# Performance work log

Hardware: AMD Instinct MI355X
Metric: run time of the kernel (lower is better)

Reference implementation:

```python
import jax, jax.numpy as jnp
import numpy as np

B, S, D, H = 4, 2048, 1024, 16
HD = D // H  # head_dim = 64


def setup_inputs() -> dict:
    key = jax.random.key(0)
    ks = jax.random.split(key, 5)
    scale = 0.02
    return {
        "x": jax.random.normal(ks[0], (B, S, D), dtype=jnp.float32),
        "Wq": jax.random.normal(ks[1], (D, D), dtype=jnp.float32) * scale,
        "Wk": jax.random.normal(ks[2], (D, D), dtype=jnp.float32) * scale,
        "Wv": jax.random.normal(ks[3], (D, D), dtype=jnp.float32) * scale,
        "Wo": jax.random.normal(ks[4], (D, D), dtype=jnp.float32) * scale,
        "bo": jnp.zeros((D,), dtype=jnp.float32),
    }


def reference(x, Wq, Wk, Wv, Wo, bo):
    b, s, d = x.shape
    # projections (no bias on q/k/v, matching qkv_bias=False)
    q = (x @ Wq).reshape(b, s, H, HD).transpose(0, 2, 1, 3)  # [B,H,S,HD]
    k = (x @ Wk).reshape(b, s, H, HD).transpose(0, 2, 1, 3)
    v = (x @ Wv).reshape(b, s, H, HD).transpose(0, 2, 1, 3)
    scores = jnp.einsum("bhqd,bhkd->bhqk", q, k) / jnp.sqrt(jnp.float32(HD))
    causal = jnp.tril(jnp.ones((s, s), dtype=bool))  # True = keep
    scores = jnp.where(causal, scores, -jnp.inf)
    attn = jax.nn.softmax(scores, axis=-1)
    # dropout p=0.0 -> identity
    out = jnp.einsum("bhqk,bhkd->bhqd", attn, v)
    out = out.transpose(0, 2, 1, 3).reshape(b, s, d)
    return out @ Wo + bo
```

## Files before the change

### kernel.cpp

```cpp
#include <hip/hip_runtime.h>

typedef unsigned short u16;
typedef unsigned int u32;
typedef __attribute__((ext_vector_type(4))) float f32x4;
typedef __attribute__((ext_vector_type(16))) float f32x16;
typedef __attribute__((ext_vector_type(8))) __bf16 bf16x8;
typedef __attribute__((ext_vector_type(4))) _Float16 f16x4;
typedef __attribute__((ext_vector_type(8))) _Float16 f16x8;
typedef __attribute__((ext_vector_type(4))) u16 u16x4;
typedef __attribute__((ext_vector_type(4))) u32 u32x4;
typedef __attribute__((ext_vector_type(2))) u32 u32x2;

#define D_ 1024
#define S_ 2048
#define B_ 4
#define H_ 16
#define HD_ 64
#define M_ 8192
#define LDP 72
#define QSCALE 0.18033688011112042591f

__device__ __forceinline__ u16 f2bf(float f) {
  u32 u = __float_as_uint(f);
  u += 0x7fffu + ((u >> 16) & 1u);
  return (u16)(u >> 16);
}

__device__ __forceinline__ float max3f(float a, float b, float c) {
  return fmaxf(fmaxf(a, b), c);
}

__device__ __forceinline__ void gload_lds16(const void* g, void* l) {
  __builtin_amdgcn_global_load_lds((const __attribute__((address_space(1))) void*)g,
                                   (__attribute__((address_space(3))) void*)l, 16, 0, 0);
}

__global__ __launch_bounds__(256) void prep_kernel(const float* __restrict__ x, u16* __restrict__ xb,
                                                   const float* __restrict__ Wq, const float* __restrict__ Wk,
                                                   const float* __restrict__ Wv, const float* __restrict__ Wo,
                                                   u16* __restrict__ Wqt, u16* __restrict__ Wkt,
                                                   u16* __restrict__ Wvt, u16* __restrict__ Wot) {
  __shared__ float lds[64][65];
  int lin = blockIdx.x;
  if (lin < 8192) {
    int i = (lin * 256 + threadIdx.x) * 4;
    f32x4 v = *(const f32x4*)(x + i);
    u16x4 o = {f2bf(v[0]), f2bf(v[1]), f2bf(v[2]), f2bf(v[3])};
    *(u16x4*)(xb + i) = o;
    return;
  }
  int pos = lin - 8192;
  int z = pos >> 8, rem = pos & 255;
  const float* W = z == 0 ? Wq : z == 1 ? Wk : z == 2 ? Wv : Wo;
  u16* Wt       = z == 0 ? Wqt : z == 1 ? Wkt : z == 2 ? Wvt : Wot;
  int k0 = (rem >> 4) * 64, n0 = (rem & 15) * 64;
  int tr = threadIdx.x >> 6, tc = threadIdx.x & 63;
#pragma unroll
  for (int i = 0; i < 16; ++i)
    lds[tr + i * 4][tc] = W[(size_t)(k0 + tr + i * 4) * D_ + n0 + tc];
  __syncthreads();
#pragma unroll
  for (int i = 0; i < 16; ++i)
    Wt[(size_t)(n0 + tr + i * 4) * D_ + k0 + tc] = f2bf(lds[tc][tr + i * 4]);
}

__device__ __forceinline__ void gemm_main(const u16* __restrict__ A, const u16* __restrict__ Bt,
                                          u16* As, u16* Bs, int row0, int col0, f32x4 acc[4][4]) {
  const int tid = threadIdx.x;
  const int lane = tid & 63, wave = tid >> 6;
  const int wr = wave >> 1, wc = wave & 1;
  const int l15 = lane & 15, lg = lane >> 4;
  const int sr8 = lane >> 3;
  const int scx = (lane & 7) ^ sr8;
#pragma unroll 1
  for (int k0 = 0; k0 < D_; k0 += 64) {
#pragma unroll
    for (int it = 0; it < 4; ++it) {
      int rbase = (it * 4 + wave) * 8;
      int r = rbase + sr8;
      gload_lds16(A + (size_t)(row0 + r) * D_ + k0 + scx * 8, As + rbase * 64);
      gload_lds16(Bt + (size_t)(col0 + r) * D_ + k0 + scx * 8, Bs + rbase * 64);
    }
    __syncthreads();
#pragma unroll
    for (int kk = 0; kk < 64; kk += 32) {
      const int cb = kk >> 3;
      bf16x8 af[4], bf[4];
#pragma unroll
      for (int m = 0; m < 4; ++m) {
        int row = wr * 64 + m * 16 + l15;
        af[m] = *(const bf16x8*)(As + row * 64 + (((cb + lg) ^ (l15 & 7)) << 3));
      }
#pragma unroll
      for (int n = 0; n < 4; ++n) {
        int row = wc * 64 + n * 16 + l15;
        bf[n] = *(const bf16x8*)(Bs + row * 64 + (((cb + lg) ^ (l15 & 7)) << 3));
      }
#pragma unroll
      for (int m = 0; m < 4; ++m)
#pragma unroll
        for (int n = 0; n < 4; ++n)
          acc[m][n] = __builtin_amdgcn_mfma_f32_16x16x32_bf16(af[m], bf[n], acc[m][n], 0, 0, 0);
    }
    __syncthreads();
  }
}

__global__ __launch_bounds__(256) void qkv_gemm_kernel(const u16* __restrict__ xb,
                                                       const u16* __restrict__ Wqt, const u16* __restrict__ Wkt,
                                                       const u16* __restrict__ Wvt,
                                                       u16* __restrict__ Qb, u16* __restrict__ Kb,
                                                       _Float16* __restrict__ Vt) {
  __shared__ u16 As[128 * 64];
  __shared__ u16 Bs[128 * 64];
  int lin = blockIdx.x;
  int xcd = lin & 7, pos = lin >> 3;
  int mode = pos / 64;
  int rem = pos & 63;
  int by = xcd * 8 + (rem >> 3);
  int bx = rem & 7;
  const u16* Bt = mode == 0 ? Wqt : mode == 1 ? Wkt : Wvt;
  f32x4 acc[4][4] = {};
  int row0 = by * 128, col0 = bx * 128;
  gemm_main(xb, Bt, As, Bs, row0, col0, acc);
  int lane = threadIdx.x & 63, wave = threadIdx.x >> 6;
  int wr = wave >> 1, wc = wave & 1, l15 = lane & 15, lg = lane >> 4;
  int rbase = row0 + wr * 64 + lg * 4, cbase = col0 + wc * 64 + l15;
  if (mode == 2) {
#pragma unroll
    for (int m = 0; m < 4; ++m) {
      int row = rbase + m * 16;
      int b = row >> 11, s = row & (S_ - 1);
#pragma unroll
      for (int n = 0; n < 4; ++n) {
        int col = cbase + n * 16;
        int h = col >> 6, hd = col & 63;
        f16x4 vv = {(_Float16)acc[m][n][0], (_Float16)acc[m][n][1],
                    (_Float16)acc[m][n][2], (_Float16)acc[m][n][3]};
        *(f16x4*)(Vt + ((size_t)((b << 4) + h) * HD_ + hd) * S_ + s) = vv;
      }
    }
  } else {
    u16* dst = mode == 0 ? Qb : Kb;
    float scl = mode == 0 ? QSCALE : 1.0f;
#pragma unroll
    for (int m = 0; m < 4; ++m)
#pragma unroll
      for (int n = 0; n < 4; ++n) {
        int col = cbase + n * 16;
#pragma unroll
        for (int r = 0; r < 4; ++r) {
          int row = rbase + m * 16 + r;
          dst[(size_t)row * D_ + col] = f2bf(acc[m][n][r] * scl);
        }
      }
  }
}

__global__ __launch_bounds__(128) void attn_kernel(const u16* __restrict__ Qb, const u16* __restrict__ Kb,
                                                   const _Float16* __restrict__ Vt, u16* __restrict__ attnb) {
  __shared__ u16 Ks[64][LDP];
  __shared__ _Float16 Vs[64][LDP];
  const int tid = threadIdx.x;
  const int wave = tid >> 6, lane = tid & 63;
  const int l31 = lane & 31, hi = lane >> 5;
  const int lin = blockIdx.x;
  const int xcd = lin & 7, slot = lin >> 3;
  const int qblk = 31 - (slot >> 3);
  const int bh = (slot & 7) * 8 + xcd;
  const int b = bh >> 4, h = bh & 15;
  const int ntiles = qblk + 1;
  const int wq0 = qblk * 64 + wave * 32;
  const int qg = wq0 + l31;

  const int srow = tid >> 1;
  const int sh = (tid & 1) * 32;
  const u16* Kp = Kb + (size_t)(b * S_ + srow) * D_ + h * HD_ + sh;
  const _Float16* Vp = Vt + ((size_t)bh * HD_ + srow) * S_ + sh;

  const u16* Qrow = Qb + (size_t)(b * S_ + qg) * D_ + h * HD_;
  bf16x8 qf[4];
#pragma unroll
  for (int ds = 0; ds < 4; ++ds)
    qf[ds] = *(const bf16x8*)(Qrow + ds * 16 + hi * 8);

  float m = -1e30f;
  f32x16 oL = {}, oH = {};
  f32x16 osum = {};
  const f16x8 ones8 = {(_Float16)1.f, (_Float16)1.f, (_Float16)1.f, (_Float16)1.f,
                       (_Float16)1.f, (_Float16)1.f, (_Float16)1.f, (_Float16)1.f};
  u32x4 kst[4], vst[4];

  auto tile_body = [&](int kvb, bool domask) {
    f32x16 sA = {}, sB = {};
    __builtin_amdgcn_s_setprio(1);
#pragma unroll
    for (int ds = 0; ds < 4; ++ds) {
      bf16x8 k0 = *(const bf16x8*)(&Ks[l31][ds * 16 + hi * 8]);
      bf16x8 k1 = *(const bf16x8*)(&Ks[32 + l31][ds * 16 + hi * 8]);
      sA = __builtin_amdgcn_mfma_f32_32x32x16_bf16(k0, qf[ds], sA, 0, 0, 0);
      sB = __builtin_amdgcn_mfma_f32_32x32x16_bf16(k1, qf[ds], sB, 0, 0, 0);
    }
    __builtin_amdgcn_s_setprio(0);
    if (domask) {
#pragma unroll
      for (int r = 0; r < 16; ++r) {
        int off = (r & 3) + 8 * (r >> 2) + 4 * hi;
        if (kvb + off > qg) sA[r] = -1e30f;
        if (kvb + 32 + off > qg) sB[r] = -1e30f;
      }
    }
    float mx[16];
#pragma unroll
    for (int r = 0; r < 16; ++r) mx[r] = fmaxf(sA[r], sB[r]);
    float y0 = max3f(mx[0], mx[1], mx[2]);
    float y1 = max3f(mx[3], mx[4], mx[5]);
    float y2 = max3f(mx[6], mx[7], mx[8]);
    float y3 = max3f(mx[9], mx[10], mx[11]);
    float y4 = max3f(mx[12], mx[13], mx[14]);
    float tmax = fmaxf(max3f(y0, y1, y2), max3f(y3, y4, mx[15]));
    tmax = fmaxf(tmax, __shfl_xor(tmax, 32));
    if (!__all(tmax - m <= 8.f)) {
      float nm = fmaxf(m, tmax);
      float alpha = exp2f(m - nm);
      m = nm;
      osum *= alpha;
      oL *= alpha;
      oH *= alpha;
    }
#pragma unroll
    for (int r = 0; r < 16; ++r) {
      sA[r] = exp2f(sA[r] - m);
      sB[r] = exp2f(sB[r] - m);
    }
    u32 uA[8], uB[8], vA[8], vB[8];
#pragma unroll
    for (int k = 0; k < 8; ++k) {
      uA[k] = __builtin_bit_cast(u32, __builtin_amdgcn_cvt_pkrtz(sA[2 * k], sA[2 * k + 1]));
      uB[k] = __builtin_bit_cast(u32, __builtin_amdgcn_cvt_pkrtz(sB[2 * k], sB[2 * k + 1]));
    }
#pragma unroll
    for (int k = 0; k < 8; ++k) {
      vA[k] = __shfl_xor(uA[k], 32);
      vB[k] = __shfl_xor(uB[k], 32);
    }
    __builtin_amdgcn_s_setprio(1);
#pragma unroll
    for (int ks = 0; ks < 4; ++ks) {
      const u32* U = (ks >> 1) ? uB : uA;
      const u32* Vw = (ks >> 1) ? vB : vA;
      const int b4 = (ks & 1) * 4;
      u32 w0 = hi ? Vw[b4 + 2] : U[b4 + 0];
      u32 w1 = hi ? Vw[b4 + 3] : U[b4 + 1];
      u32 w2 = hi ? U[b4 + 2] : Vw[b4 + 0];
      u32 w3 = hi ? U[b4 + 3] : Vw[b4 + 1];
      f16x8 pa = __builtin_bit_cast(f16x8, (u32x4){w0, w1, w2, w3});
      f16x8 v0 = *(const f16x8*)(&Vs[l31][ks * 16 + hi * 8]);
      f16x8 v1 = *(const f16x8*)(&Vs[32 + l31][ks * 16 + hi * 8]);
      oL = __builtin_amdgcn_mfma_f32_32x32x16_f16(v0, pa, oL, 0, 0, 0);
      oH = __builtin_amdgcn_mfma_f32_32x32x16_f16(v1, pa, oH, 0, 0, 0);
      osum = __builtin_amdgcn_mfma_f32_32x32x16_f16(ones8, pa, osum, 0, 0, 0);
    }
    __builtin_amdgcn_s_setprio(0);
  };

#pragma unroll
  for (int c = 0; c < 4; ++c) {
    kst[c] = *(const u32x4*)(Kp + c * 8);
    vst[c] = *(const u32x4*)(Vp + c * 8);
  }
  Kp += (size_t)64 * D_;
  Vp += 64;

#pragma unroll 1
  for (int t = 0; t < ntiles - 1; ++t) {
    __syncthreads();
#pragma unroll
    for (int c = 0; c < 4; ++c) {
      *(u32x4*)(&Ks[srow][sh + c * 8]) = kst[c];
      *(u32x4*)(&Vs[srow][sh + c * 8]) = vst[c];
    }
    __syncthreads();
#pragma unroll
    for (int c = 0; c < 4; ++c) {
      kst[c] = *(const u32x4*)(Kp + c * 8);
      vst[c] = *(const u32x4*)(Vp + c * 8);
    }
    Kp += (size_t)64 * D_;
    Vp += 64;
    tile_body(t * 64, false);
  }

  __syncthreads();
#pragma unroll
  for (int c = 0; c < 4; ++c) {
    *(u32x4*)(&Ks[srow][sh + c * 8]) = kst[c];
    *(u32x4*)(&Vs[srow][sh + c * 8]) = vst[c];
  }
  __syncthreads();
  tile_body((ntiles - 1) * 64, true);

  float inv = 1.0f / osum[0];
  __syncthreads();
  u16* scr = &Ks[wave * 32 + l31][0];
#pragma unroll
  for (int a = 0; a < 4; ++a) {
    u16x4 pl = {f2bf(oL[4 * a + 0] * inv), f2bf(oL[4 * a + 1] * inv),
                f2bf(oL[4 * a + 2] * inv), f2bf(oL[4 * a + 3] * inv)};
    *(u16x4*)(scr + 8 * a + 4 * hi) = pl;
    u16x4 ph = {f2bf(oH[4 * a + 0] * inv), f2bf(oH[4 * a + 1] * inv),
                f2bf(oH[4 * a + 2] * inv), f2bf(oH[4 * a + 3] * inv)};
    *(u16x4*)(scr + 32 + 8 * a + 4 * hi) = ph;
  }
  asm volatile("s_waitcnt lgkmcnt(0)" ::: "memory");
  const u16* srd = &Ks[wave * 32 + l31][hi * 32];
  u16* Og = attnb + (size_t)(b * S_ + wq0 + l31) * D_ + h * HD_ + hi * 32;
#pragma unroll
  for (int c = 0; c < 4; ++c)
    *(u32x4*)(Og + c * 8) = *(const u32x4*)(srd + c * 8);
}

__global__ __launch_bounds__(256) void out_gemm_kernel(const u16* __restrict__ attnb, const u16* __restrict__ Wot,
                                                       const float* __restrict__ bo, float* __restrict__ outp) {
  __shared__ u16 As[128 * 64];
  __shared__ u16 Bs[128 * 64];
  int lin = blockIdx.x;
  int xcd = lin & 7, pos = lin >> 3;
  int by = xcd * 8 + (pos >> 3);
  int bx = pos & 7;
  f32x4 acc[4][4] = {};
  int row0 = by * 128, col0 = bx * 128;
  gemm_main(attnb, Wot, As, Bs, row0, col0, acc);
  int lane = threadIdx.x & 63, wave = threadIdx.x >> 6;
  int wr = wave >> 1, wc = wave & 1, l15 = lane & 15, lg = lane >> 4;
  int rbase = row0 + wr * 64 + lg * 4, cbase = col0 + wc * 64 + l15;
#pragma unroll
  for (int n = 0; n < 4; ++n) {
    float bn = bo[cbase + n * 16];
#pragma unroll
    for (int m = 0; m < 4; ++m)
#pragma unroll
      for (int r = 0; r < 4; ++r)
        outp[(size_t)(rbase + m * 16 + r) * D_ + cbase + n * 16] = acc[m][n][r] + bn;
  }
}

extern "C" void kernel_launch(void* const* d_in, const int* in_sizes, int n_in,
                              void* d_out, int out_size, void* d_ws, size_t ws_size,
                              hipStream_t stream) {
  const float* x  = (const float*)d_in[0];
  const float* Wq = (const float*)d_in[1];
  const float* Wk = (const float*)d_in[2];
  const float* Wv = (const float*)d_in[3];
  const float* Wo = (const float*)d_in[4];
  const float* bo = (const float*)d_in[5];
  float* outp = (float*)d_out;

  char* ws = (char*)d_ws;
  u16* xb        = (u16*)(ws);
  u16* Wqt       = (u16*)(ws + ((size_t)16 << 20));
  u16* Wkt       = (u16*)(ws + ((size_t)18 << 20));
  u16* Wvt       = (u16*)(ws + ((size_t)20 << 20));
  u16* Wot       = (u16*)(ws + ((size_t)22 << 20));
  u16* Qb        = (u16*)(ws + ((size_t)24 << 20));
  u16* Kb        = (u16*)(ws + ((size_t)40 << 20));
  _Float16* Vt   = (_Float16*)(ws + ((size_t)56 << 20));
  u16* attnb     = (u16*)(ws + ((size_t)72 << 20));

  prep_kernel<<<dim3(9216), dim3(256), 0, stream>>>(x, xb, Wq, Wk, Wv, Wo, Wqt, Wkt, Wvt, Wot);
  qkv_gemm_kernel<<<dim3(1536), dim3(256), 0, stream>>>(xb, Wqt, Wkt, Wvt, Qb, Kb, Vt);
  attn_kernel<<<dim3(2048), dim3(128), 0, stream>>>(Qb, Kb, Vt, attnb);
  out_gemm_kernel<<<dim3(512), dim3(256), 0, stream>>>(attnb, Wot, bo, outp);
}
```

Measured before the change: 184.7 us.

## Use 128-query attention blocks with four waves sharing each K/V tile

The attention kernel now processes 128 query rows per block with 256 threads (four waves) instead of 64 rows with two waves. Each K/V tile is loaded into shared memory once and reused by twice as many query waves, which halves global K/V traffic per query. Waves whose diagonal tile comes earlier skip the tiles past it. The cost is idle waves on the last causal tile (imbalance within a block), fewer blocks in the grid, and the output staging now spans both the Ks and Vs buffers.

Result: slower. 188.9 us (+2.3%).

```diff
diff --git a/kernel.cpp b/kernel.cpp
--- a/kernel.cpp
+++ b/kernel.cpp
@@ -157,7 +157,7 @@
   }
 }
 
-__global__ __launch_bounds__(128) void attn_kernel(const u16* __restrict__ Qb, const u16* __restrict__ Kb,
+__global__ __launch_bounds__(256) void attn_kernel(const u16* __restrict__ Qb, const u16* __restrict__ Kb,
                                                    const _Float16* __restrict__ Vt, u16* __restrict__ attnb) {
   __shared__ u16 Ks[64][LDP];
   __shared__ _Float16 Vs[64][LDP];
@@ -166,17 +166,18 @@
   const int l31 = lane & 31, hi = lane >> 5;
   const int lin = blockIdx.x;
   const int xcd = lin & 7, slot = lin >> 3;
-  const int qblk = 31 - (slot >> 3);
+  const int qblk = 15 - (slot >> 3);
   const int bh = (slot & 7) * 8 + xcd;
   const int b = bh >> 4, h = bh & 15;
-  const int ntiles = qblk + 1;
-  const int wq0 = qblk * 64 + wave * 32;
+  const int ntiles = 2 * qblk + 2;
+  const int wq0 = qblk * 128 + wave * 32;
   const int qg = wq0 + l31;
-
-  const int srow = tid >> 1;
-  const int sh = (tid & 1) * 32;
-  const u16* Kp = Kb + (size_t)(b * S_ + srow) * D_ + h * HD_ + sh;
-  const _Float16* Vp = Vt + ((size_t)bh * HD_ + srow) * S_ + sh;
+  const int tdiag = wq0 >> 6;
+
+  const int srow = tid >> 2;
+  const int sc = (tid & 3) * 16;
+  const u16* Kp = Kb + (size_t)(b * S_ + srow) * D_ + h * HD_ + sc;
+  const _Float16* Vp = Vt + ((size_t)bh * HD_ + srow) * S_ + sc;
 
   const u16* Qrow = Qb + (size_t)(b * S_ + qg) * D_ + h * HD_;
   bf16x8 qf[4];
@@ -189,7 +190,7 @@
   f32x16 osum = {};
   const f16x8 ones8 = {(_Float16)1.f, (_Float16)1.f, (_Float16)1.f, (_Float16)1.f,
                        (_Float16)1.f, (_Float16)1.f, (_Float16)1.f, (_Float16)1.f};
-  u32x4 kst[4], vst[4];
+  u32x4 kst0, kst1, vst0, vst1;
 
   auto tile_body = [&](int kvb, bool domask) {
     f32x16 sA = {}, sB = {};
@@ -264,45 +265,41 @@
     __builtin_amdgcn_s_setprio(0);
   };
 
-#pragma unroll
-  for (int c = 0; c < 4; ++c) {
-    kst[c] = *(const u32x4*)(Kp + c * 8);
-    vst[c] = *(const u32x4*)(Vp + c * 8);
-  }
+  kst0 = *(const u32x4*)(Kp);
+  kst1 = *(const u32x4*)(Kp + 8);
+  vst0 = *(const u32x4*)(Vp);
+  vst1 = *(const u32x4*)(Vp + 8);
   Kp += (size_t)64 * D_;
   Vp += 64;
 
 #pragma unroll 1
   for (int t = 0; t < ntiles - 1; ++t) {
     __syncthreads();
-#pragma unroll
-    for (int c = 0; c < 4; ++c) {
-      *(u32x4*)(&Ks[srow][sh + c * 8]) = kst[c];
-      *(u32x4*)(&Vs[srow][sh + c * 8]) = vst[c];
-    }
+    *(u32x4*)(&Ks[srow][sc]) = kst0;
+    *(u32x4*)(&Ks[srow][sc + 8]) = kst1;
+    *(u32x4*)(&Vs[srow][sc]) = vst0;
+    *(u32x4*)(&Vs[srow][sc + 8]) = vst1;
     __syncthreads();
-#pragma unroll
-    for (int c = 0; c < 4; ++c) {
-      kst[c] = *(const u32x4*)(Kp + c * 8);
-      vst[c] = *(const u32x4*)(Vp + c * 8);
-    }
+    kst0 = *(const u32x4*)(Kp);
+    kst1 = *(const u32x4*)(Kp + 8);
+    vst0 = *(const u32x4*)(Vp);
+    vst1 = *(const u32x4*)(Vp + 8);
     Kp += (size_t)64 * D_;
     Vp += 64;
-    tile_body(t * 64, false);
+    if (t <= tdiag) tile_body(t * 64, t == tdiag);
   }
 
   __syncthreads();
-#pragma unroll
-  for (int c = 0; c < 4; ++c) {
-    *(u32x4*)(&Ks[srow][sh + c * 8]) = kst[c];
-    *(u32x4*)(&Vs[srow][sh + c * 8]) = vst[c];
-  }
+  *(u32x4*)(&Ks[srow][sc]) = kst0;
+  *(u32x4*)(&Ks[srow][sc + 8]) = kst1;
+  *(u32x4*)(&Vs[srow][sc]) = vst0;
+  *(u32x4*)(&Vs[srow][sc + 8]) = vst1;
   __syncthreads();
-  tile_body((ntiles - 1) * 64, true);
+  if (tdiag == ntiles - 1) tile_body((ntiles - 1) * 64, true);
 
   float inv = 1.0f / osum[0];
   __syncthreads();
-  u16* scr = &Ks[wave * 32 + l31][0];
+  u16* scr = (wave < 2) ? &Ks[wave * 32 + l31][0] : (u16*)&Vs[(wave - 2) * 32 + l31][0];
 #pragma unroll
   for (int a = 0; a < 4; ++a) {
     u16x4 pl = {f2bf(oL[4 * a + 0] * inv), f2bf(oL[4 * a + 1] * inv),
@@ -313,7 +310,7 @@
     *(u16x4*)(scr + 32 + 8 * a + 4 * hi) = ph;
   }
   asm volatile("s_waitcnt lgkmcnt(0)" ::: "memory");
-  const u16* srd = &Ks[wave * 32 + l31][hi * 32];
+  const u16* srd = ((wave < 2) ? &Ks[wave * 32 + l31][0] : (u16*)&Vs[(wave - 2) * 32 + l31][0]) + hi * 32;
   u16* Og = attnb + (size_t)(b * S_ + wq0 + l31) * D_ + h * HD_ + hi * 32;
 #pragma unroll
   for (int c = 0; c < 4; ++c)
@@ -369,6 +366,6 @@
 
   prep_kernel<<<dim3(9216), dim3(256), 0, stream>>>(x, xb, Wq, Wk, Wv, Wo, Wqt, Wkt, Wvt, Wot);
   qkv_gemm_kernel<<<dim3(1536), dim3(256), 0, stream>>>(xb, Wqt, Wkt, Wvt, Qb, Kb, Vt);
-  attn_kernel<<<dim3(2048), dim3(128), 0, stream>>>(Qb, Kb, Vt, attnb);
+  attn_kernel<<<dim3(1024), dim3(256), 0, stream>>>(Qb, Kb, Vt, attnb);
   out_gemm_kernel<<<dim3(512), dim3(256), 0, stream>>>(attnb, Wot, bo, outp);
 }
```
